# Performance work log

Measured on AMD Instinct MI355X. Metric: run time of the kernel, lower is better.

The kernel has to match this reference:

```python
import jax, jax.numpy as jnp
import numpy as np
from jax import lax

K = 9      # 3x3 kernel points
PAD = 1
EPS = 1e-5

def _conv3x3(x, w):
    # x: [B,C,H,W], w: [O,C,3,3] -> [B,O,H,W], stride 1, pad 1
    return lax.conv_general_dilated(x, w, (1, 1), [(PAD, PAD), (PAD, PAD)],
                                    dimension_numbers=('NCHW', 'OIHW', 'NCHW'))

def _bilinear_sample(x, py, px):
    # x: [B,C,H,W]; py,px: [B,K,H,W] float sample coords -> [B,C,K,H,W]
    # Zero padding outside bounds (mmcv deform_conv semantics).
    B, C, H, W = x.shape
    y0 = jnp.floor(py)
    x0 = jnp.floor(px)
    wy1 = py - y0
    wx1 = px - x0
    xf = x.reshape(B, C, H * W)

    def corner(yc, xc, wgt):
        valid = (yc >= 0) & (yc <= H - 1) & (xc >= 0) & (xc <= W - 1)
        yi = jnp.clip(yc, 0, H - 1).astype(jnp.int32)
        xi = jnp.clip(xc, 0, W - 1).astype(jnp.int32)
        idx = (yi * W + xi).reshape(B, -1)                       # [B, K*H*W]
        v = jax.vmap(lambda f, i: jnp.take(f, i, axis=1))(xf, idx)  # [B,C,K*H*W]
        v = v.reshape(B, C, K, H, W)
        return v * jnp.where(valid, wgt, 0.0)[:, None]

    return (corner(y0,     x0,     (1 - wy1) * (1 - wx1))
          + corner(y0,     x0 + 1, (1 - wy1) * wx1)
          + corner(y0 + 1, x0,     wy1 * (1 - wx1))
          + corner(y0 + 1, x0 + 1, wy1 * wx1))

def _dcn_bn_relu(x, w_off, b_off, w, gamma, beta, mean, var):
    B, C, H, W = x.shape
    # offset conv: [B, 2K, H, W]; channel pairs are (dy, dx) per kernel point
    off = _conv3x3(x, w_off) + b_off[None, :, None, None]
    off = off.reshape(B, K, 2, H, W)
    dy, dx = off[:, :, 0], off[:, :, 1]
    kk = jnp.arange(K)
    ky = (kk // 3 - PAD).astype(x.dtype)   # kernel y deltas
    kx = (kk % 3 - PAD).astype(x.dtype)    # kernel x deltas
    py = dy + jnp.arange(H, dtype=x.dtype)[None, None, :, None] + ky[None, :, None, None]
    px = dx + jnp.arange(W, dtype=x.dtype)[None, None, None, :] + kx[None, :, None, None]
    s = _bilinear_sample(x, py, px)                       # [B,C,K,H,W]
    out = jnp.einsum('bckhw,ock->bohw', s, w.reshape(w.shape[0], C, K))
    # BatchNorm (eval stats) + ReLU
    inv = gamma * lax.rsqrt(var + EPS)
    return jax.nn.relu(out * inv[None, :, None, None]
                       + (beta - mean * inv)[None, :, None, None])

def setup_inputs() -> dict:
    key = jax.random.key(0)
    ks = jax.random.split(key, 8)
    B, Cin, Cout, H, W = 4, 64, 64, 128, 128
    fan = 1.0 / np.sqrt(Cin * K)
    return {
        'x':      jax.random.normal(ks[0], (B, Cin, H, W), jnp.float32),
        'w_off1': jax.random.normal(ks[1], (2 * K, Cin, 3, 3), jnp.float32) * 0.1,
        'b_off1': jnp.zeros((2 * K,), jnp.float32),
        'w1':     jax.random.normal(ks[2], (Cout, Cin, 3, 3), jnp.float32) * fan,
        'g1':     jnp.ones((Cout,), jnp.float32),
        'be1':    jnp.zeros((Cout,), jnp.float32),
        'm1':     jax.random.normal(ks[3], (Cout,), jnp.float32) * 0.01,
        'v1':     jnp.abs(jax.random.normal(ks[4], (Cout,), jnp.float32)) * 0.1 + 0.9,
        'w_off2': jax.random.normal(ks[5], (2 * K, Cout, 3, 3), jnp.float32) * 0.1,
        'b_off2': jnp.zeros((2 * K,), jnp.float32),
        'w2':     jax.random.normal(ks[6], (Cout, Cout, 3, 3), jnp.float32) * fan,
        'g2':     jnp.ones((Cout,), jnp.float32),
        'be2':    jnp.zeros((Cout,), jnp.float32),
        'm2':     jax.random.normal(ks[7], (Cout,), jnp.float32) * 0.01,
        'v2':     jnp.ones((Cout,), jnp.float32),
    }

def reference(x, w_off1, b_off1, w1, g1, be1, m1, v1,
              w_off2, b_off2, w2, g2, be2, m2, v2):
    h = _dcn_bn_relu(x, w_off1, b_off1, w1, g1, be1, m1, v1)
    return _dcn_bn_relu(h, w_off2, b_off2, w2, g2, be2, m2, v2)
```

## Files before the change

### kernel.cpp

```cpp
#include <hip/hip_runtime.h>

#define BAR_LGKM()                                         \
  do {                                                     \
    asm volatile("s_waitcnt lgkmcnt(0)" ::: "memory");     \
    __builtin_amdgcn_s_barrier();                          \
  } while (0)


__global__ __launch_bounds__(256) void prep_kernel(
    const float* __restrict__ w1, const float* __restrict__ w2,
    const float* __restrict__ woff1, const float* __restrict__ woff2,
    const float* __restrict__ g1, const float* __restrict__ be1,
    const float* __restrict__ m1, const float* __restrict__ v1,
    const float* __restrict__ g2, const float* __restrict__ be2,
    const float* __restrict__ m2, const float* __restrict__ v2,
    float* __restrict__ ws) {
  float* wt1 = ws;
  float* wt2 = ws + 36864;
  float* wo1 = ws + 73728;
  float* wo2 = ws + 84096;
  float* bn1 = ws + 94464;
  float* bn2 = ws + 94592;
  int idx = blockIdx.x * 256 + threadIdx.x;
  if (idx < 73728) {
    int t = (idx < 36864) ? idx : idx - 36864;
    const float* w = (idx < 36864) ? w1 : w2;
    float* wt = (idx < 36864) ? wt1 : wt2;
    int oi = t & 7;
    int rest = t >> 3;
    int k = rest % 9;
    int cog = rest / 9;
    int og = cog & 7, c = cog >> 3;
    int o = og * 8 + oi;
    wt[t] = w[(o * 64 + c) * 9 + k];
  } else if (idx < 94464) {
    int u = idx - 73728;
    int t2 = (u < 10368) ? u : u - 10368;
    const float* w = (u < 10368) ? woff1 : woff2;
    float* wo = (u < 10368) ? wo1 : wo2;
    int j = t2 % 18;
    int v = t2 / 18;
    int tt = v % 9;
    int c = v / 9;
    wo[t2] = w[(j * 64 + c) * 9 + tt];
  } else if (idx < 94528) {
    int o = idx - 94464;
    float s = g1[o] * rsqrtf(v1[o] + 1e-5f);
    bn1[o] = s;
    bn1[64 + o] = be1[o] - m1[o] * s;
  } else if (idx < 94592) {
    int o = idx - 94528;
    float s = g2[o] * rsqrtf(v2[o] + 1e-5f);
    bn2[o] = s;
    bn2[64 + o] = be2[o] - m2[o] * s;
  }
}

__global__ __launch_bounds__(512, 8) void conv_off_kernel(
    const float* __restrict__ xin, const float* __restrict__ wofft,
    const float* __restrict__ boff, float* __restrict__ off) {
  __shared__ float halo[2][396];
  int tid = threadIdx.x;
  int pxl = tid & 63;
  int og = tid >> 6;
  int ogu = __builtin_amdgcn_readfirstlane(og);
  int p0 = blockIdx.x * 64;
  int b = p0 >> 14, hw0 = p0 & 16383;
  int h = hw0 >> 7, w0 = hw0 & 127;

  bool sv = tid < 396;
  int pl = (tid >= 198) ? 1 : 0;
  int pos = tid - pl * 198;
  int r = pos / 66, cc = pos - r * 66;
  int yy = h + r - 1, xx = w0 + cc - 1;
  bool inb = sv && (yy >= 0) && (yy < 128) && (xx >= 0) && (xx < 128);
  int ofs = ((pl << 14) + (yy << 7)) + xx;
  const float* xb0 = xin + ((size_t)(b * 64) << 14);

  float stg = inb ? xb0[ofs] : 0.f;

  int jbase = (ogu < 2) ? ogu * 3 : 6 + (ogu - 2) * 2;
  int nj = (ogu < 2) ? 3 : 2;
  int jc2 = jbase + 2;
  if (jc2 > 17) jc2 = 17;

  float acc[3] = {0.f, 0.f, 0.f};

#pragma unroll 1
  for (int c = 0; c < 64; c += 2) {
    if (sv) halo[(c >> 1) & 1][tid] = stg;
    if (c < 62) stg = inb ? xb0[((size_t)(c + 2) << 14) + ofs] : 0.f;
    BAR_LGKM();
    const float* hb = halo[(c >> 1) & 1];
#pragma unroll
    for (int p = 0; p < 2; ++p) {
      const float* wc = wofft + (c + p) * 162;
#pragma unroll
      for (int t = 0; t < 9; ++t) {
        float v = hb[p * 198 + (t / 3) * 66 + pxl + (t % 3)];
        acc[0] = fmaf(v, wc[t * 18 + jbase], acc[0]);
        acc[1] = fmaf(v, wc[t * 18 + jbase + 1], acc[1]);
        acc[2] = fmaf(v, wc[t * 18 + jc2], acc[2]);
      }
    }
  }
#pragma unroll
  for (int i = 0; i < 3; ++i) {
    if (i < nj) {
      int j = jbase + i;
      off[((size_t)(b * 18 + j) << 14) + hw0 + pxl] = acc[i] + boff[j];
    }
  }
}

__global__ __launch_bounds__(512, 8) void dcn_main_kernel(
    const float* __restrict__ xin, const float* __restrict__ off,
    const float* __restrict__ wt, const float* __restrict__ bn,
    float* __restrict__ out) {
  __shared__ float sbuf[2][576];
  int tid = threadIdx.x;
  int pxl = tid & 63;
  int og = tid >> 6;
  int ogu = __builtin_amdgcn_readfirstlane(og);
  int p0 = blockIdx.x * 64;
  int b = p0 >> 14, hw0 = p0 & 16383;
  int h = hw0 >> 7, w0 = hw0 & 127;
  const float* xb = xin + ((size_t)b << 20);

  bool act1 = (tid & 7) == 0;
  int s1 = 512 + (tid >> 3);

  float pw0[4], pw1[4];
  int ra0, rb0, ra1, rb1;
  bool se0a, se1a, se0b, se1b;

#pragma unroll
  for (int j = 0; j < 2; ++j) {
    bool a = (j == 0) || act1;
    int s = (j == 0) ? tid : s1;
    int k = s >> 6;
    int pxs = s & 63;
    int hw = hw0 + pxs;
    float dy = a ? off[((size_t)(b * 18 + 2 * k) << 14) + hw] : 0.f;
    float dx = a ? off[((size_t)(b * 18 + 2 * k + 1) << 14) + hw] : 0.f;
    float py = (float)(h + k / 3 - 1) + dy;
    float pxf = (float)(w0 + pxs + k % 3 - 1) + dx;
    float y0f = floorf(py), x0f = floorf(pxf);
    float wy1 = py - y0f, wx1 = pxf - x0f;
    float wy0 = 1.f - wy1, wx0 = 1.f - wx1;
    int y0 = (int)y0f, x0 = (int)x0f;
    int y1 = y0 + 1, x1 = x0 + 1;
    bool vy0 = (y0 >= 0) && (y0 <= 127);
    bool vy1 = (y1 >= 0) && (y1 <= 127);
    bool vx0 = (x0 >= 0) && (x0 <= 127);
    bool vx1 = (x1 >= 0) && (x1 <= 127);
    float* pw = (j == 0) ? pw0 : pw1;
    pw[0] = (vy0 && vx0) ? wy0 * wx0 : 0.f;
    pw[1] = (vy0 && vx1) ? wy0 * wx1 : 0.f;
    pw[2] = (vy1 && vx0) ? wy1 * wx0 : 0.f;
    pw[3] = (vy1 && vx1) ? wy1 * wx1 : 0.f;
    int y0c = min(max(y0, 0), 127), y1c = min(max(y1, 0), 127);
    int xb2 = min(max(x0, 0), 126);
    if (j == 0) {
      ra0 = (y0c << 7) + xb2; rb0 = (y1c << 7) + xb2;
      se0a = (x0 == xb2); se1a = (x0 + 1 == xb2);
    } else {
      ra1 = (y0c << 7) + xb2; rb1 = (y1c << 7) + xb2;
      se0b = (x0 == xb2); se1b = (x0 + 1 == xb2);
    }
  }

  float2 t0a, t1a, t0b, t1b;
  t0a = *(const float2*)(xb + ra0);
  t1a = *(const float2*)(xb + rb0);
  t0b = act1 ? *(const float2*)(xb + ra1) : make_float2(0.f, 0.f);
  t1b = act1 ? *(const float2*)(xb + rb1) : make_float2(0.f, 0.f);

  float acc[8];
#pragma unroll
  for (int oi = 0; oi < 8; ++oi) acc[oi] = 0.f;

#pragma unroll 1
  for (int c = 0; c < 64; ++c) {
    {
      float v00 = se0a ? t0a.x : t0a.y;
      float v01 = se1a ? t0a.x : t0a.y;
      float v10 = se0a ? t1a.x : t1a.y;
      float v11 = se1a ? t1a.x : t1a.y;
      sbuf[c & 1][tid] = fmaf(pw0[0], v00,
                         fmaf(pw0[1], v01,
                         fmaf(pw0[2], v10, pw0[3] * v11)));
    }
    if (act1) {
      float v00 = se0b ? t0b.x : t0b.y;
      float v01 = se1b ? t0b.x : t0b.y;
      float v10 = se0b ? t1b.x : t1b.y;
      float v11 = se1b ? t1b.x : t1b.y;
      sbuf[c & 1][s1] = fmaf(pw1[0], v00,
                        fmaf(pw1[1], v01,
                        fmaf(pw1[2], v10, pw1[3] * v11)));
    }
    if (c < 63) {
      const float* xn = xb + ((size_t)(c + 1) << 14);
      t0a = *(const float2*)(xn + ra0);
      t1a = *(const float2*)(xn + rb0);
      if (act1) {
        t0b = *(const float2*)(xn + ra1);
        t1b = *(const float2*)(xn + rb1);
      }
    }
    BAR_LGKM();
    const float* wc = wt + (c * 8 + ogu) * 72;
#pragma unroll
    for (int k = 0; k < 9; ++k) {
      float sval = sbuf[c & 1][k * 64 + pxl];
#pragma unroll
      for (int oi = 0; oi < 8; ++oi)
        acc[oi] = fmaf(sval, wc[k * 8 + oi], acc[oi]);
    }
  }

#pragma unroll
  for (int oi = 0; oi < 8; ++oi) {
    int o = ogu * 8 + oi;
    float rres = fmaf(acc[oi], bn[o], bn[64 + o]);
    out[((size_t)(b * 64 + o) << 14) + hw0 + pxl] = fmaxf(rres, 0.f);
  }
}

extern "C" void kernel_launch(void* const* d_in, const int* in_sizes, int n_in,
                              void* d_out, int out_size, void* d_ws, size_t ws_size,
                              hipStream_t stream) {
  const float* x      = (const float*)d_in[0];
  const float* w_off1 = (const float*)d_in[1];
  const float* b_off1 = (const float*)d_in[2];
  const float* w1     = (const float*)d_in[3];
  const float* g1     = (const float*)d_in[4];
  const float* be1    = (const float*)d_in[5];
  const float* m1     = (const float*)d_in[6];
  const float* v1     = (const float*)d_in[7];
  const float* w_off2 = (const float*)d_in[8];
  const float* b_off2 = (const float*)d_in[9];
  const float* w2     = (const float*)d_in[10];
  const float* g2     = (const float*)d_in[11];
  const float* be2    = (const float*)d_in[12];
  const float* m2     = (const float*)d_in[13];
  const float* v2     = (const float*)d_in[14];
  float* out = (float*)d_out;

  float* ws   = (float*)d_ws;
  float* wt1  = ws;
  float* wt2  = ws + 36864;
  float* wo1  = ws + 73728;
  float* wo2  = ws + 84096;
  float* bn1  = ws + 94464;
  float* bn2  = ws + 94592;
  float* offb = ws + 94720;
  float* hbuf = ws + 1274368;

  prep_kernel<<<370, 256, 0, stream>>>(w1, w2, w_off1, w_off2,
                                       g1, be1, m1, v1, g2, be2, m2, v2, ws);

  conv_off_kernel<<<1024, 512, 0, stream>>>(x, wo1, b_off1, offb);
  dcn_main_kernel<<<1024, 512, 0, stream>>>(x, offb, wt1, bn1, hbuf);

  conv_off_kernel<<<1024, 512, 0, stream>>>(hbuf, wo2, b_off2, offb);
  dcn_main_kernel<<<1024, 512, 0, stream>>>(hbuf, offb, wt2, bn2, out);
}
```

Before: 376.1 us.

## Deepen gather prefetch, stage four channels per halo, and swizzle block order

The deformable gather loop now prefetches two channels ahead, using two register sets that alternate with the two LDS buffers. This gives global loads more time in flight before the barrier that consumes them. The offset conv stages four input channels per halo fill, which halves the number of barriers. Both kernels remap block indices so that consecutive blocks land on different image rows or batches, changing cache and channel locality. The cost is more live registers under an 8-waves occupancy bound and a larger LDS footprint in the offset conv.

```diff
diff --git a/kernel.cpp b/kernel.cpp
--- a/kernel.cpp
+++ b/kernel.cpp
@@ -5,6 +5,10 @@
     asm volatile("s_waitcnt lgkmcnt(0)" ::: "memory");     \
     __builtin_amdgcn_s_barrier();                          \
   } while (0)
+
+__device__ __forceinline__ int swz_block(int bid) {
+  return ((bid & 7) << 7) + (bid >> 3);
+}
 
 
 __global__ __launch_bounds__(256) void prep_kernel(
@@ -59,25 +63,26 @@
 __global__ __launch_bounds__(512, 8) void conv_off_kernel(
     const float* __restrict__ xin, const float* __restrict__ wofft,
     const float* __restrict__ boff, float* __restrict__ off) {
-  __shared__ float halo[2][396];
+  __shared__ float halo[2][792];
   int tid = threadIdx.x;
   int pxl = tid & 63;
   int og = tid >> 6;
   int ogu = __builtin_amdgcn_readfirstlane(og);
-  int p0 = blockIdx.x * 64;
+  int p0 = swz_block(blockIdx.x) * 64;
   int b = p0 >> 14, hw0 = p0 & 16383;
   int h = hw0 >> 7, w0 = hw0 & 127;
 
   bool sv = tid < 396;
-  int pl = (tid >= 198) ? 1 : 0;
-  int pos = tid - pl * 198;
+  int pp = (tid >= 198) ? 1 : 0;
+  int pos = tid - pp * 198;
   int r = pos / 66, cc = pos - r * 66;
   int yy = h + r - 1, xx = w0 + cc - 1;
   bool inb = sv && (yy >= 0) && (yy < 128) && (xx >= 0) && (xx < 128);
-  int ofs = ((pl << 14) + (yy << 7)) + xx;
+  int ofs = (yy << 7) + xx;
   const float* xb0 = xin + ((size_t)(b * 64) << 14);
 
-  float stg = inb ? xb0[ofs] : 0.f;
+  float stg0 = inb ? xb0[((size_t)pp << 14) + ofs] : 0.f;
+  float stg1 = inb ? xb0[((size_t)(2 + pp) << 14) + ofs] : 0.f;
 
   int jbase = (ogu < 2) ? ogu * 3 : 6 + (ogu - 2) * 2;
   int nj = (ogu < 2) ? 3 : 2;
@@ -87,14 +92,21 @@
   float acc[3] = {0.f, 0.f, 0.f};
 
 #pragma unroll 1
-  for (int c = 0; c < 64; c += 2) {
-    if (sv) halo[(c >> 1) & 1][tid] = stg;
-    if (c < 62) stg = inb ? xb0[((size_t)(c + 2) << 14) + ofs] : 0.f;
+  for (int cg = 0; cg < 64; cg += 4) {
+    int bufi = (cg >> 2) & 1;
+    if (sv) {
+      halo[bufi][pp * 198 + pos] = stg0;
+      halo[bufi][(2 + pp) * 198 + pos] = stg1;
+    }
+    if (cg < 60) {
+      stg0 = inb ? xb0[((size_t)(cg + 4 + pp) << 14) + ofs] : 0.f;
+      stg1 = inb ? xb0[((size_t)(cg + 6 + pp) << 14) + ofs] : 0.f;
+    }
     BAR_LGKM();
-    const float* hb = halo[(c >> 1) & 1];
-#pragma unroll
-    for (int p = 0; p < 2; ++p) {
-      const float* wc = wofft + (c + p) * 162;
+    const float* hb = halo[bufi];
+#pragma unroll
+    for (int p = 0; p < 4; ++p) {
+      const float* wc = wofft + (cg + p) * 162;
 #pragma unroll
       for (int t = 0; t < 9; ++t) {
         float v = hb[p * 198 + (t / 3) * 66 + pxl + (t % 3)];
@@ -122,7 +134,7 @@
   int pxl = tid & 63;
   int og = tid >> 6;
   int ogu = __builtin_amdgcn_readfirstlane(og);
-  int p0 = blockIdx.x * 64;
+  int p0 = swz_block(blockIdx.x) * 64;
   int b = p0 >> 14, hw0 = p0 & 16383;
   int h = hw0 >> 7, w0 = hw0 & 127;
   const float* xb = xin + ((size_t)b << 20);
@@ -170,53 +182,100 @@
     }
   }
 
-  float2 t0a, t1a, t0b, t1b;
-  t0a = *(const float2*)(xb + ra0);
-  t1a = *(const float2*)(xb + rb0);
-  t0b = act1 ? *(const float2*)(xb + ra1) : make_float2(0.f, 0.f);
-  t1b = act1 ? *(const float2*)(xb + rb1) : make_float2(0.f, 0.f);
+  float2 A0, A1, A2, A3, B0, B1, B2, B3;
+  A0 = *(const float2*)(xb + ra0);
+  A1 = *(const float2*)(xb + rb0);
+  A2 = act1 ? *(const float2*)(xb + ra1) : make_float2(0.f, 0.f);
+  A3 = act1 ? *(const float2*)(xb + rb1) : make_float2(0.f, 0.f);
+  {
+    const float* x1p = xb + 16384;
+    B0 = *(const float2*)(x1p + ra0);
+    B1 = *(const float2*)(x1p + rb0);
+    B2 = act1 ? *(const float2*)(x1p + ra1) : make_float2(0.f, 0.f);
+    B3 = act1 ? *(const float2*)(x1p + rb1) : make_float2(0.f, 0.f);
+  }
 
   float acc[8];
 #pragma unroll
   for (int oi = 0; oi < 8; ++oi) acc[oi] = 0.f;
 
 #pragma unroll 1
-  for (int c = 0; c < 64; ++c) {
+  for (int c = 0; c < 64; c += 2) {
     {
-      float v00 = se0a ? t0a.x : t0a.y;
-      float v01 = se1a ? t0a.x : t0a.y;
-      float v10 = se0a ? t1a.x : t1a.y;
-      float v11 = se1a ? t1a.x : t1a.y;
-      sbuf[c & 1][tid] = fmaf(pw0[0], v00,
-                         fmaf(pw0[1], v01,
-                         fmaf(pw0[2], v10, pw0[3] * v11)));
+      float v00 = se0a ? A0.x : A0.y;
+      float v01 = se1a ? A0.x : A0.y;
+      float v10 = se0a ? A1.x : A1.y;
+      float v11 = se1a ? A1.x : A1.y;
+      sbuf[0][tid] = fmaf(pw0[0], v00,
+                     fmaf(pw0[1], v01,
+                     fmaf(pw0[2], v10, pw0[3] * v11)));
     }
     if (act1) {
-      float v00 = se0b ? t0b.x : t0b.y;
-      float v01 = se1b ? t0b.x : t0b.y;
-      float v10 = se0b ? t1b.x : t1b.y;
-      float v11 = se1b ? t1b.x : t1b.y;
-      sbuf[c & 1][s1] = fmaf(pw1[0], v00,
-                        fmaf(pw1[1], v01,
-                        fmaf(pw1[2], v10, pw1[3] * v11)));
-    }
-    if (c < 63) {
-      const float* xn = xb + ((size_t)(c + 1) << 14);
-      t0a = *(const float2*)(xn + ra0);
-      t1a = *(const float2*)(xn + rb0);
+      float v00 = se0b ? A2.x : A2.y;
+      float v01 = se1b ? A2.x : A2.y;
+      float v10 = se0b ? A3.x : A3.y;
+      float v11 = se1b ? A3.x : A3.y;
+      sbuf[0][s1] = fmaf(pw1[0], v00,
+                    fmaf(pw1[1], v01,
+                    fmaf(pw1[2], v10, pw1[3] * v11)));
+    }
+    if (c < 62) {
+      const float* xn = xb + ((size_t)(c + 2) << 14);
+      A0 = *(const float2*)(xn + ra0);
+      A1 = *(const float2*)(xn + rb0);
       if (act1) {
-        t0b = *(const float2*)(xn + ra1);
-        t1b = *(const float2*)(xn + rb1);
+        A2 = *(const float2*)(xn + ra1);
+        A3 = *(const float2*)(xn + rb1);
       }
     }
     BAR_LGKM();
-    const float* wc = wt + (c * 8 + ogu) * 72;
-#pragma unroll
-    for (int k = 0; k < 9; ++k) {
-      float sval = sbuf[c & 1][k * 64 + pxl];
-#pragma unroll
-      for (int oi = 0; oi < 8; ++oi)
-        acc[oi] = fmaf(sval, wc[k * 8 + oi], acc[oi]);
+    {
+      const float* wc = wt + (c * 8 + ogu) * 72;
+#pragma unroll
+      for (int k = 0; k < 9; ++k) {
+        float sval = sbuf[0][k * 64 + pxl];
+#pragma unroll
+        for (int oi = 0; oi < 8; ++oi)
+          acc[oi] = fmaf(sval, wc[k * 8 + oi], acc[oi]);
+      }
+    }
+    {
+      float v00 = se0a ? B0.x : B0.y;
+      float v01 = se1a ? B0.x : B0.y;
+      float v10 = se0a ? B1.x : B1.y;
+      float v11 = se1a ? B1.x : B1.y;
+      sbuf[1][tid] = fmaf(pw0[0], v00,
+                     fmaf(pw0[1], v01,
+                     fmaf(pw0[2], v10, pw0[3] * v11)));
+    }
+    if (act1) {
+      float v00 = se0b ? B2.x : B2.y;
+      float v01 = se1b ? B2.x : B2.y;
+      float v10 = se0b ? B3.x : B3.y;
+      float v11 = se1b ? B3.x : B3.y;
+      sbuf[1][s1] = fmaf(pw1[0], v00,
+                    fmaf(pw1[1], v01,
+                    fmaf(pw1[2], v10, pw1[3] * v11)));
+    }
+    if (c < 61) {
+      const float* xn = xb + ((size_t)(c + 3) << 14);
+      B0 = *(const float2*)(xn + ra0);
+      B1 = *(const float2*)(xn + rb0);
+      if (act1) {
+        B2 = *(const float2*)(xn + ra1);
+        B3 = *(const float2*)(xn + rb1);
+      }
+    }
+    BAR_LGKM();
+    {
+      const float* wc = wt + ((c + 1) * 8 + ogu) * 72;
+#pragma unroll
+      for (int k = 0; k < 9; ++k) {
+        float sval = sbuf[1][k * 64 + pxl];
+#pragma unroll
+        for (int oi = 0; oi < 8; ++oi)
+          acc[oi] = fmaf(sval, wc[k * 8 + oi], acc[oi]);
+      }
     }
   }
 
```

Result: slower. 386.9 us (+2.9%).

## Swizzle block order, stage four channels per barrier, fold bilinear selects into weights

Applied to the files above, without the earlier changes.

Adds a block-index swizzle to both conv kernels, so consecutive blocks map to rows 128 blocks apart instead of adjacent pixel tiles. The offset conv now stages four channels per iteration into a larger shared halo, which halves the number of barriers. The deformable kernel folds the per-corner x-select logic into four precomputed weights and walks the input with advancing pointers, removing per-channel selects and address arithmetic. The swizzle changes cache locality in ways that may help or hurt, and the larger halo and extra staging registers could affect occupancy.

```diff
diff --git a/kernel.cpp b/kernel.cpp
--- a/kernel.cpp
+++ b/kernel.cpp
@@ -5,6 +5,10 @@
     asm volatile("s_waitcnt lgkmcnt(0)" ::: "memory");     \
     __builtin_amdgcn_s_barrier();                          \
   } while (0)
+
+__device__ __forceinline__ int swz_block(int bid) {
+  return ((bid & 7) << 7) + (bid >> 3);
+}
 
 
 __global__ __launch_bounds__(256) void prep_kernel(
@@ -59,25 +63,26 @@
 __global__ __launch_bounds__(512, 8) void conv_off_kernel(
     const float* __restrict__ xin, const float* __restrict__ wofft,
     const float* __restrict__ boff, float* __restrict__ off) {
-  __shared__ float halo[2][396];
+  __shared__ float halo[2][792];
   int tid = threadIdx.x;
   int pxl = tid & 63;
   int og = tid >> 6;
   int ogu = __builtin_amdgcn_readfirstlane(og);
-  int p0 = blockIdx.x * 64;
+  int p0 = swz_block(blockIdx.x) * 64;
   int b = p0 >> 14, hw0 = p0 & 16383;
   int h = hw0 >> 7, w0 = hw0 & 127;
 
   bool sv = tid < 396;
-  int pl = (tid >= 198) ? 1 : 0;
-  int pos = tid - pl * 198;
+  int pp = (tid >= 198) ? 1 : 0;
+  int pos = tid - pp * 198;
   int r = pos / 66, cc = pos - r * 66;
   int yy = h + r - 1, xx = w0 + cc - 1;
   bool inb = sv && (yy >= 0) && (yy < 128) && (xx >= 0) && (xx < 128);
-  int ofs = ((pl << 14) + (yy << 7)) + xx;
+  int ofs = (yy << 7) + xx;
   const float* xb0 = xin + ((size_t)(b * 64) << 14);
 
-  float stg = inb ? xb0[ofs] : 0.f;
+  float stg0 = inb ? xb0[((size_t)pp << 14) + ofs] : 0.f;
+  float stg1 = inb ? xb0[((size_t)(2 + pp) << 14) + ofs] : 0.f;
 
   int jbase = (ogu < 2) ? ogu * 3 : 6 + (ogu - 2) * 2;
   int nj = (ogu < 2) ? 3 : 2;
@@ -87,14 +92,21 @@
   float acc[3] = {0.f, 0.f, 0.f};
 
 #pragma unroll 1
-  for (int c = 0; c < 64; c += 2) {
-    if (sv) halo[(c >> 1) & 1][tid] = stg;
-    if (c < 62) stg = inb ? xb0[((size_t)(c + 2) << 14) + ofs] : 0.f;
+  for (int cg = 0; cg < 64; cg += 4) {
+    int bufi = (cg >> 2) & 1;
+    if (sv) {
+      halo[bufi][pp * 198 + pos] = stg0;
+      halo[bufi][(2 + pp) * 198 + pos] = stg1;
+    }
+    if (cg < 60) {
+      stg0 = inb ? xb0[((size_t)(cg + 4 + pp) << 14) + ofs] : 0.f;
+      stg1 = inb ? xb0[((size_t)(cg + 6 + pp) << 14) + ofs] : 0.f;
+    }
     BAR_LGKM();
-    const float* hb = halo[(c >> 1) & 1];
-#pragma unroll
-    for (int p = 0; p < 2; ++p) {
-      const float* wc = wofft + (c + p) * 162;
+    const float* hb = halo[bufi];
+#pragma unroll
+    for (int p = 0; p < 4; ++p) {
+      const float* wc = wofft + (cg + p) * 162;
 #pragma unroll
       for (int t = 0; t < 9; ++t) {
         float v = hb[p * 198 + (t / 3) * 66 + pxl + (t % 3)];
@@ -122,7 +134,7 @@
   int pxl = tid & 63;
   int og = tid >> 6;
   int ogu = __builtin_amdgcn_readfirstlane(og);
-  int p0 = blockIdx.x * 64;
+  int p0 = swz_block(blockIdx.x) * 64;
   int b = p0 >> 14, hw0 = p0 & 16383;
   int h = hw0 >> 7, w0 = hw0 & 127;
   const float* xb = xin + ((size_t)b << 20);
@@ -130,9 +142,9 @@
   bool act1 = (tid & 7) == 0;
   int s1 = 512 + (tid >> 3);
 
-  float pw0[4], pw1[4];
-  int ra0, rb0, ra1, rb1;
-  bool se0a, se1a, se0b, se1b;
+  float q[2][4];
+  const float* pa[2];
+  const float* pb[2];
 
 #pragma unroll
   for (int j = 0; j < 2; ++j) {
@@ -154,27 +166,27 @@
     bool vy1 = (y1 >= 0) && (y1 <= 127);
     bool vx0 = (x0 >= 0) && (x0 <= 127);
     bool vx1 = (x1 >= 0) && (x1 <= 127);
-    float* pw = (j == 0) ? pw0 : pw1;
-    pw[0] = (vy0 && vx0) ? wy0 * wx0 : 0.f;
-    pw[1] = (vy0 && vx1) ? wy0 * wx1 : 0.f;
-    pw[2] = (vy1 && vx0) ? wy1 * wx0 : 0.f;
-    pw[3] = (vy1 && vx1) ? wy1 * wx1 : 0.f;
+    float pw0 = (vy0 && vx0) ? wy0 * wx0 : 0.f;
+    float pw1 = (vy0 && vx1) ? wy0 * wx1 : 0.f;
+    float pw2 = (vy1 && vx0) ? wy1 * wx0 : 0.f;
+    float pw3 = (vy1 && vx1) ? wy1 * wx1 : 0.f;
     int y0c = min(max(y0, 0), 127), y1c = min(max(y1, 0), 127);
     int xb2 = min(max(x0, 0), 126);
-    if (j == 0) {
-      ra0 = (y0c << 7) + xb2; rb0 = (y1c << 7) + xb2;
-      se0a = (x0 == xb2); se1a = (x0 + 1 == xb2);
-    } else {
-      ra1 = (y0c << 7) + xb2; rb1 = (y1c << 7) + xb2;
-      se0b = (x0 == xb2); se1b = (x0 + 1 == xb2);
-    }
-  }
-
-  float2 t0a, t1a, t0b, t1b;
-  t0a = *(const float2*)(xb + ra0);
-  t1a = *(const float2*)(xb + rb0);
-  t0b = act1 ? *(const float2*)(xb + ra1) : make_float2(0.f, 0.f);
-  t1b = act1 ? *(const float2*)(xb + rb1) : make_float2(0.f, 0.f);
+    bool se0 = (x0 == xb2);
+    bool se1 = (x0 + 1 == xb2);
+    q[j][0] = (se0 ? pw0 : 0.f) + (se1 ? pw1 : 0.f);
+    q[j][1] = (se0 ? 0.f : pw0) + (se1 ? 0.f : pw1);
+    q[j][2] = (se0 ? pw2 : 0.f) + (se1 ? pw3 : 0.f);
+    q[j][3] = (se0 ? 0.f : pw2) + (se1 ? 0.f : pw3);
+    pa[j] = xb + ((y0c << 7) + xb2);
+    pb[j] = xb + ((y1c << 7) + xb2);
+  }
+
+  float2 t0a = *(const float2*)pa[0];
+  float2 t1a = *(const float2*)pb[0];
+  float2 t0b = act1 ? *(const float2*)pa[1] : make_float2(0.f, 0.f);
+  float2 t1b = act1 ? *(const float2*)pb[1] : make_float2(0.f, 0.f);
+  pa[0] += 16384; pb[0] += 16384; pa[1] += 16384; pb[1] += 16384;
 
   float acc[8];
 #pragma unroll
@@ -182,32 +194,22 @@
 
 #pragma unroll 1
   for (int c = 0; c < 64; ++c) {
-    {
-      float v00 = se0a ? t0a.x : t0a.y;
-      float v01 = se1a ? t0a.x : t0a.y;
-      float v10 = se0a ? t1a.x : t1a.y;
-      float v11 = se1a ? t1a.x : t1a.y;
-      sbuf[c & 1][tid] = fmaf(pw0[0], v00,
-                         fmaf(pw0[1], v01,
-                         fmaf(pw0[2], v10, pw0[3] * v11)));
-    }
+    sbuf[c & 1][tid] = fmaf(q[0][0], t0a.x,
+                       fmaf(q[0][1], t0a.y,
+                       fmaf(q[0][2], t1a.x, q[0][3] * t1a.y)));
     if (act1) {
-      float v00 = se0b ? t0b.x : t0b.y;
-      float v01 = se1b ? t0b.x : t0b.y;
-      float v10 = se0b ? t1b.x : t1b.y;
-      float v11 = se1b ? t1b.x : t1b.y;
-      sbuf[c & 1][s1] = fmaf(pw1[0], v00,
-                        fmaf(pw1[1], v01,
-                        fmaf(pw1[2], v10, pw1[3] * v11)));
+      sbuf[c & 1][s1] = fmaf(q[1][0], t0b.x,
+                        fmaf(q[1][1], t0b.y,
+                        fmaf(q[1][2], t1b.x, q[1][3] * t1b.y)));
     }
     if (c < 63) {
-      const float* xn = xb + ((size_t)(c + 1) << 14);
-      t0a = *(const float2*)(xn + ra0);
-      t1a = *(const float2*)(xn + rb0);
+      t0a = *(const float2*)pa[0];
+      t1a = *(const float2*)pb[0];
       if (act1) {
-        t0b = *(const float2*)(xn + ra1);
-        t1b = *(const float2*)(xn + rb1);
+        t0b = *(const float2*)pa[1];
+        t1b = *(const float2*)pb[1];
       }
+      pa[0] += 16384; pb[0] += 16384; pa[1] += 16384; pb[1] += 16384;
     }
     BAR_LGKM();
     const float* wc = wt + (c * 8 + ogu) * 72;
```

After: 375.5 us. Within noise of the previous version (-0.2%).
